# Kernel tuning notes

Hardware: AMD Instinct MI355X
Metric: run time of the kernel (lower is better)

## Reference

```python
import jax, jax.numpy as jnp
import numpy as np

N = 100000          # nodes
E = 1600000         # directed edges (avg degree 16)
DIMS = [256, 256, 256, 128]


def setup_inputs() -> dict:
    key = jax.random.key(0)
    ks = jax.random.split(key, 3 + 2 * (len(DIMS) - 1))
    X = jax.random.normal(ks[0], (N, DIMS[0]), dtype=jnp.float32)
    row = jax.random.randint(ks[1], (E,), 0, N, dtype=jnp.int32)
    col = jax.random.randint(ks[2], (E,), 0, N, dtype=jnp.int32)
    inp = {"X": X, "row": row, "col": col}
    # LinearLayer params: weights ~ N(0,1)/sqrt(in_features), bias = 0
    for i in range(len(DIMS) - 1):
        d_in, d_out = DIMS[i], DIMS[i + 1]
        inp[f"W{i}"] = jax.random.normal(ks[3 + i], (d_out, d_in), dtype=jnp.float32) / jnp.sqrt(d_in)
        inp[f"b{i}"] = jnp.zeros((d_out,), dtype=jnp.float32)
    return inp


def reference(X, row, col, W0, b0, W1, b1, W2, b2):
    n = X.shape[0]
    # normalized_adjacency: A' = I + A, then D^{-1/2} A' D^{-1/2}
    loop = jnp.arange(n, dtype=row.dtype)
    rows = jnp.concatenate([row, loop])          # [E+N]
    cols = jnp.concatenate([col, loop])          # [E+N]
    vals = jnp.ones(rows.shape[0], dtype=X.dtype)
    deg = jax.ops.segment_sum(vals, rows, num_segments=n)   # row sums of A'
    norm = vals / (jnp.sqrt(deg[rows]) * jnp.sqrt(deg[cols]))  # [E+N]

    def spmm(H):  # S @ H via gather + scatter-add
        return jax.ops.segment_sum(norm[:, None] * H[cols], rows, num_segments=n)

    H = spmm(X)
    H = jax.nn.gelu(H @ W0.T + b0)
    H = spmm(H)
    H = jax.nn.gelu(H @ W1.T + b1)
    H = spmm(H)
    H = H @ W2.T + b2  # final_non_linearity = identity
    return H
```

## Files before the change

### kernel.cpp

```cpp
#include <hip/hip_runtime.h>
#include <hip/hip_bf16.h>


typedef float f32x4 __attribute__((ext_vector_type(4)));
typedef float f32x2 __attribute__((ext_vector_type(2)));
typedef _Float16 h16x8 __attribute__((ext_vector_type(8)));
typedef _Float16 h16x4 __attribute__((ext_vector_type(4)));

__device__ __forceinline__ float gelu_fast(float x) {
    float u = 0.7978845608028654f * (x + 0.044715f * x * x * x);
    return x / (1.0f + __expf(-2.0f * u));
}

__global__ void count_kernel(const int* __restrict__ row, int* __restrict__ cnt,
                             int* __restrict__ rank, int e) {
    int i = blockIdx.x * blockDim.x + threadIdx.x;
    if (i < e) rank[i] = atomicAdd(&cnt[row[i]], 1);
}

__global__ void rnorm_kernel(const int* __restrict__ cnt, float* __restrict__ rnorm, int n) {
    int i = blockIdx.x * blockDim.x + threadIdx.x;
    if (i < n) rnorm[i] = rsqrtf((float)(cnt[i] + 1));
}

__global__ void scan1_kernel(const int* __restrict__ cnt, int* __restrict__ rowptr,
                             int* __restrict__ bsum, int n) {
    __shared__ int s[1024];
    int t = threadIdx.x;
    int i = blockIdx.x * 1024 + t;
    int v = (i < n) ? cnt[i] : 0;
    s[t] = v;
    __syncthreads();
    for (int off = 1; off < 1024; off <<= 1) {
        int x = (t >= off) ? s[t - off] : 0;
        __syncthreads();
        s[t] += x;
        __syncthreads();
    }
    if (i < n) rowptr[i] = s[t] - v;
    if (t == 1023) bsum[blockIdx.x] = s[1023];
}

__global__ void scan2_kernel(int* bsum, int nb) {
    __shared__ int s[128];
    int t = threadIdx.x;
    int v = (t < nb) ? bsum[t] : 0;
    s[t] = v;
    __syncthreads();
    for (int off = 1; off < 128; off <<= 1) {
        int x = (t >= off) ? s[t - off] : 0;
        __syncthreads();
        s[t] += x;
        __syncthreads();
    }
    if (t < nb) bsum[t] = s[t] - v;
}

__global__ void scan3_kernel(int* __restrict__ rowptr, const int* __restrict__ bsum, int n, int e) {
    int i = blockIdx.x * blockDim.x + threadIdx.x;
    if (i < n) rowptr[i] += bsum[i >> 10];
    if (i == 0) rowptr[n] = e;
}

__global__ void fill_kernel(const int* __restrict__ row, const int* __restrict__ col,
                            const int* __restrict__ rank,
                            const int* __restrict__ rowptr,
                            const float* __restrict__ rnorm,
                            int2* __restrict__ meta, int e) {
    int i = blockIdx.x * blockDim.x + threadIdx.x;
    if (i >= e) return;
    int r = row[i], c = col[i];
    int pos = rowptr[r] + rank[i];
    float w = rnorm[r] * rnorm[c];
    meta[pos] = make_int2(c, __float_as_int(w));
}

__global__ void splitW_kernel(const float* __restrict__ in,
                              _Float16* __restrict__ hi,
                              _Float16* __restrict__ lo, int total4) {
    int i = blockIdx.x * blockDim.x + threadIdx.x;
    if (i >= total4) return;
    f32x4 x = *(const f32x4*)(in + (size_t)i * 4);
    h16x4 h, l;
#pragma unroll
    for (int q = 0; q < 4; ++q) {
        _Float16 hb = (_Float16)x[q];
        h[q] = hb;
        l[q] = (_Float16)(x[q] - (float)hb);
    }
    *(h16x4*)(hi + (size_t)i * 4) = h;
    *(h16x4*)(lo + (size_t)i * 4) = l;
}

template <int D, bool GELU, bool SPLIT>
__global__ __launch_bounds__(256) void spmm_kernel(const _Float16* __restrict__ in,
                                                   float* __restrict__ out,
                                                   _Float16* __restrict__ oat,
                                                   const int* __restrict__ rowptr,
                                                   const int2* __restrict__ meta,
                                                   const float* __restrict__ rnorm,
                                                   const float* __restrict__ bias, int n) {
    constexpr int LPR = D / 8;
    constexpr int RPW = 64 / LPR;
    constexpr int BR = 4 * RPW;
    __shared__ _Float16 h_lds[8][256];

    int t = threadIdx.x;
    int lane = t & 63;
    int w = t >> 6;
    int sub = lane % LPR;
    int rowsel = lane / LPR;
    int wid = blockIdx.x * BR + w * RPW + rowsel;
    if (wid >= n) wid = n - 1;

    const _Float16* lanebase = in + sub * 8;
    float rn = rnorm[wid];
    float sw = rn * rn;
    float acc[8];
    {
        h16x8 a = *(const h16x8*)(lanebase + (size_t)wid * D);
#pragma unroll
        for (int q = 0; q < 8; ++q) acc[q] = sw * (float)a[q];
    }

    int e0 = rowptr[wid], e1 = rowptr[wid + 1];
    int ne = e1 - e0;
    int maxb = (ne + 3) >> 2;
    int elast = (e1 > e0) ? (e1 - 1) : 0;

    int2 m[4];
    auto loadM = [&](int b) {
#pragma unroll
        for (int u = 0; u < 4; ++u) {
            int idx = e0 + b * 4 + u;
            int eu = idx < e1 ? idx : elast;
            int2 mm = meta[eu];
            if (idx >= e1) mm.y = 0;
            m[u] = mm;
        }
    };
    if (maxb > 0) loadM(0);
    for (int b = 0; b < maxb; ++b) {
        h16x8 v[4];
#pragma unroll
        for (int u = 0; u < 4; ++u)
            v[u] = *(const h16x8*)(lanebase + (size_t)m[u].x * D);
        float wts[4];
#pragma unroll
        for (int u = 0; u < 4; ++u) wts[u] = __int_as_float(m[u].y);
        if (b + 1 < maxb) loadM(b + 1);
#pragma unroll
        for (int u = 0; u < 4; ++u)
#pragma unroll
            for (int q = 0; q < 8; ++q) acc[q] = fmaf(wts[u], (float)v[u][q], acc[q]);
    }

    if (SPLIT) {
        f32x4 bv0 = *(const f32x4*)(bias + sub * 8);
        f32x4 bv1 = *(const f32x4*)(bias + sub * 8 + 4);
        h16x8 h;
#pragma unroll
        for (int q = 0; q < 4; ++q) {
            float x0 = acc[q] + bv0[q];
            float x1 = acc[q + 4] + bv1[q];
            h[q] = (_Float16)(GELU ? gelu_fast(x0) : x0);
            h[q + 4] = (_Float16)(GELU ? gelu_fast(x1) : x1);
        }
        *(h16x8*)&h_lds[w * 2 + rowsel][sub * 8] = h;
        __syncthreads();
        int kc = t >> 5;
        int g  = (t >> 3) & 3;
        int j  = t & 7;
        size_t rg = (size_t)(blockIdx.x >> 1);
        int half = blockIdx.x & 1;
        size_t toff = ((rg * 8 + kc) * 64 + g * 16 + half * 8 + j) * 8;
        __builtin_nontemporal_store(*(const h16x8*)&h_lds[j][kc * 32 + g * 8],
                                    (h16x8*)(oat + toff));
    } else {
        f32x4 bv0 = *(const f32x4*)(bias + sub * 8);
        f32x4 bv1 = *(const f32x4*)(bias + sub * 8 + 4);
        f32x4 o0, o1;
#pragma unroll
        for (int q = 0; q < 4; ++q) {
            float x0 = acc[q] + bv0[q];
            float x1 = acc[q + 4] + bv1[q];
            o0[q] = GELU ? gelu_fast(x0) : x0;
            o1[q] = GELU ? gelu_fast(x1) : x1;
        }
        float* dst = out + (size_t)wid * D + sub * 8;
        __builtin_nontemporal_store(o0, (f32x4*)dst);
        __builtin_nontemporal_store(o1, (f32x4*)(dst + 4));
    }
}

template <int DO, int RT, bool XIN>
__global__ __launch_bounds__(256, 2) void dense_mfma_kernel(
        const _Float16* __restrict__ AT, const float* __restrict__ Xf,
        const _Float16* __restrict__ Whi, const _Float16* __restrict__ Wlo,
        _Float16* __restrict__ out, int n) {
    constexpr int KC = 32;
    constexpr int NCH = 256 / KC;
    constexpr int NTT = DO / 16;
    constexpr int NT = NTT / 2;
    constexpr int NFRAG = 2 * NTT;
    constexpr int BM = 2 * RT * 16;
    __shared__ h16x8 s_w[2][NFRAG * 64];

    int t = threadIdx.x;
    int lane = t & 63;
    int w = t >> 6;
    int r = lane & 15;
    int g = lane >> 4;
    int h = w & 1;
    int row0 = blockIdx.x * BM + (w >> 1) * (RT * 16);
    int n16 = (n + 15) >> 4;

    size_t argi[RT];
#pragma unroll
    for (int rt = 0; rt < RT; ++rt) {
        if (XIN) {
            int arow = row0 + rt * 16 + r;
            if (arow >= n) arow = n - 1;
            argi[rt] = (size_t)arow;
        } else {
            int rg = (row0 >> 4) + rt;
            if (rg >= n16) rg = n16 - 1;
            argi[rt] = (size_t)rg;
        }
    }

    f32x4 acc[RT][NT];
#pragma unroll
    for (int rt = 0; rt < RT; ++rt)
#pragma unroll
        for (int nt = 0; nt < NT; ++nt) acc[rt][nt] = (f32x4){0.f, 0.f, 0.f, 0.f};

    auto stage = [&](int c, int b) {
#pragma unroll
        for (int i = 0; i < NFRAG / 4; ++i) {
            int s = t + i * 256;
            int sl = s & 63;
            int f = s >> 6;
            int ntf = f % NTT;
            int op = f / NTT;
            const _Float16* src = op ? Wlo : Whi;
            const _Float16* gsrc =
                &src[(size_t)(ntf * 16 + (sl & 15)) * 256 + c * KC + ((sl >> 4) << 3)];
            __builtin_amdgcn_global_load_lds(
                (const __attribute__((address_space(1))) void*)gsrc,
                (__attribute__((address_space(3))) void*)&s_w[b][s], 16, 0, 0);
        }
    };

    h16x8 aC[2][RT];
    f32x4 nf[RT][2];

    auto prefetchA = [&](int c, int set) {
#pragma unroll
        for (int rt = 0; rt < RT; ++rt) {
            if (XIN) {
                const float* src = &Xf[argi[rt] * 256 + c * KC + g * 8];
                nf[rt][0] = *(const f32x4*)src;
                nf[rt][1] = *(const f32x4*)(src + 4);
            } else {
                aC[set][rt] = *(const h16x8*)&AT[((argi[rt] * 8 + c) * 64 + lane) * 8];
            }
        }
    };
    auto commitA = [&](int set) {
        if (XIN) {
#pragma unroll
            for (int rt = 0; rt < RT; ++rt) {
                h16x8 hh;
#pragma unroll
                for (int q = 0; q < 4; ++q) {
                    hh[q] = (_Float16)nf[rt][0][q];
                    hh[q + 4] = (_Float16)nf[rt][1][q];
                }
                aC[set][rt] = hh;
            }
        }
    };

    stage(0, 0);
    prefetchA(0, 0);
    asm volatile("s_waitcnt vmcnt(0)" ::: "memory");
    __builtin_amdgcn_sched_barrier(0);
    commitA(0);
    __builtin_amdgcn_s_barrier();
    __builtin_amdgcn_sched_barrier(0);

#pragma unroll
    for (int c = 0; c < NCH; ++c) {
        const int b = c & 1;
        if (c + 1 < NCH) {
            stage(c + 1, b ^ 1);
            prefetchA(c + 1, b ^ 1);
            constexpr int VM = (NFRAG / 4) + (XIN ? 2 * RT : RT);
            asm volatile("s_waitcnt vmcnt(%0)" :: "i"(VM) : "memory");
        } else {
            asm volatile("s_waitcnt vmcnt(0)" ::: "memory");
        }
        __builtin_amdgcn_sched_barrier(0);
        __builtin_amdgcn_s_barrier();
        __builtin_amdgcn_sched_barrier(0);

#pragma unroll
        for (int nt = 0; nt < NT; ++nt) {
            int ntf = h * NT + nt;
            h16x8 wh = s_w[b][ntf * 64 + lane];
            h16x8 wl = s_w[b][(NTT + ntf) * 64 + lane];
#pragma unroll
            for (int rt = 0; rt < RT; ++rt) {
                acc[rt][nt] = __builtin_amdgcn_mfma_f32_16x16x32_f16(aC[b][rt], wh, acc[rt][nt], 0, 0, 0);
                acc[rt][nt] = __builtin_amdgcn_mfma_f32_16x16x32_f16(aC[b][rt], wl, acc[rt][nt], 0, 0, 0);
            }
        }
        __builtin_amdgcn_sched_barrier(0);
        if (c + 1 < NCH) commitA(b ^ 1);
        __builtin_amdgcn_s_barrier();
    }

#pragma unroll
    for (int rt = 0; rt < RT; ++rt) {
#pragma unroll
        for (int nt = 0; nt < NT; ++nt) {
            int ccol = (h * NT + nt) * 16 + r;
#pragma unroll
            for (int j = 0; j < 4; ++j) {
                int rr = row0 + rt * 16 + g * 4 + j;
                if (rr < n) out[(size_t)rr * DO + ccol] = (_Float16)acc[rt][nt][j];
            }
        }
    }
}

extern "C" void kernel_launch(void* const* d_in, const int* in_sizes, int n_in,
                              void* d_out, int out_size, void* d_ws, size_t ws_size,
                              hipStream_t stream) {
    const float* X  = (const float*)d_in[0];
    const int* row  = (const int*)d_in[1];
    const int* col  = (const int*)d_in[2];
    const float* W0 = (const float*)d_in[3];
    const float* b0 = (const float*)d_in[4];
    const float* W1 = (const float*)d_in[5];
    const float* b1 = (const float*)d_in[6];
    const float* W2 = (const float*)d_in[7];
    const float* b2 = (const float*)d_in[8];

    int n = in_sizes[0] / 256;
    int e = in_sizes[1];
    size_t n16pad = (size_t)((n + 15) / 16) * 16;

    char* ws = (char*)d_ws;
    size_t off = 0;
    auto alloc = [&](size_t bytes) {
        void* p = ws + off;
        off += (bytes + 255) & ~(size_t)255;
        return p;
    };
    _Float16* AT  = (_Float16*)alloc(n16pad * 256 * 2);
    _Float16* Dh  = (_Float16*)alloc((size_t)n * 256 * 2);
    _Float16* W0h = (_Float16*)alloc(256 * 256 * 2);
    _Float16* W0l = (_Float16*)alloc(256 * 256 * 2);
    _Float16* W1h = (_Float16*)alloc(256 * 256 * 2);
    _Float16* W1l = (_Float16*)alloc(256 * 256 * 2);
    _Float16* W2h = (_Float16*)alloc(256 * 128 * 2);
    _Float16* W2l = (_Float16*)alloc(256 * 128 * 2);
    int*   cnt    = (int*)alloc((size_t)n * 4);
    int*   rank   = (int*)alloc((size_t)e * 4);
    float* rnorm  = (float*)alloc((size_t)n * 4);
    int*   rowptr = (int*)alloc(((size_t)n + 1) * 4);
    int*   bsum   = (int*)alloc(512);
    int2*  meta   = (int2*)alloc((size_t)e * 8);

    (void)hipMemsetAsync(cnt, 0, (size_t)n * 4, stream);

    int gE = (e + 255) / 256;
    int gN = (n + 255) / 256;
    int nb = (n + 1023) / 1024;

    count_kernel<<<gE, 256, 0, stream>>>(row, cnt, rank, e);
    rnorm_kernel<<<gN, 256, 0, stream>>>(cnt, rnorm, n);
    scan1_kernel<<<nb, 1024, 0, stream>>>(cnt, rowptr, bsum, n);
    scan2_kernel<<<1, 128, 0, stream>>>(bsum, nb);
    scan3_kernel<<<gN, 256, 0, stream>>>(rowptr, bsum, n, e);
    fill_kernel<<<gE, 256, 0, stream>>>(row, col, rank, rowptr, rnorm, meta, e);

    splitW_kernel<<<(16384 + 255) / 256, 256, 0, stream>>>(W0, W0h, W0l, 16384);
    splitW_kernel<<<(16384 + 255) / 256, 256, 0, stream>>>(W1, W1h, W1l, 16384);
    splitW_kernel<<<(8192 + 255) / 256, 256, 0, stream>>>(W2, W2h, W2l, 8192);

    int gS  = (n + 7) / 8;
    int gS2 = (n + 15) / 16;
    int gMd = (n + 127) / 128;

    dense_mfma_kernel<256, 4, true><<<gMd, 256, 0, stream>>>(nullptr, X, W0h, W0l, Dh, n);
    spmm_kernel<256, true, true><<<gS, 256, 0, stream>>>(Dh, nullptr, AT, rowptr, meta, rnorm, b0, n);
    dense_mfma_kernel<256, 4, false><<<gMd, 256, 0, stream>>>(AT, nullptr, W1h, W1l, Dh, n);
    spmm_kernel<256, true, true><<<gS, 256, 0, stream>>>(Dh, nullptr, AT, rowptr, meta, rnorm, b1, n);
    dense_mfma_kernel<128, 4, false><<<gMd, 256, 0, stream>>>(AT, nullptr, W2h, W2l, Dh, n);
    spmm_kernel<128, false, false><<<gS2, 256, 0, stream>>>(Dh, (float*)d_out, nullptr, rowptr, meta, rnorm, b2, n);
}
```

Before: 574.0 us.

## Factor symmetric normalization out of edges, store only column indices

Splits the edge weight rnorm[r]*rnorm[c] so the column factor is applied in the dense GEMM epilogue and the row factor in the SpMM epilogue. The per-edge metadata shrinks from an int2 (column plus weight) to a bare column index, halving metadata traffic in each SpMM. The rnorm computation moves into scan1 and the three weight-split launches merge into one, removing several small launches. Padding is added to rnorm and AT so the vectorized rnorm read past n stays in bounds, and results change slightly because fp16 values are now rounded after scaling.

```diff
diff --git a/kernel.cpp b/kernel.cpp
--- a/kernel.cpp
+++ b/kernel.cpp
@@ -18,17 +18,13 @@
     if (i < e) rank[i] = atomicAdd(&cnt[row[i]], 1);
 }
 
-__global__ void rnorm_kernel(const int* __restrict__ cnt, float* __restrict__ rnorm, int n) {
-    int i = blockIdx.x * blockDim.x + threadIdx.x;
-    if (i < n) rnorm[i] = rsqrtf((float)(cnt[i] + 1));
-}
-
 __global__ void scan1_kernel(const int* __restrict__ cnt, int* __restrict__ rowptr,
-                             int* __restrict__ bsum, int n) {
+                             int* __restrict__ bsum, float* __restrict__ rnorm, int n) {
     __shared__ int s[1024];
     int t = threadIdx.x;
     int i = blockIdx.x * 1024 + t;
     int v = (i < n) ? cnt[i] : 0;
+    if (i < n) rnorm[i] = rsqrtf((float)(v + 1));
     s[t] = v;
     __syncthreads();
     for (int off = 1; off < 1024; off <<= 1) {
@@ -65,22 +61,25 @@
 __global__ void fill_kernel(const int* __restrict__ row, const int* __restrict__ col,
                             const int* __restrict__ rank,
                             const int* __restrict__ rowptr,
-                            const float* __restrict__ rnorm,
-                            int2* __restrict__ meta, int e) {
+                            int* __restrict__ metac, int e) {
     int i = blockIdx.x * blockDim.x + threadIdx.x;
     if (i >= e) return;
-    int r = row[i], c = col[i];
-    int pos = rowptr[r] + rank[i];
-    float w = rnorm[r] * rnorm[c];
-    meta[pos] = make_int2(c, __float_as_int(w));
-}
-
-__global__ void splitW_kernel(const float* __restrict__ in,
-                              _Float16* __restrict__ hi,
-                              _Float16* __restrict__ lo, int total4) {
+    metac[rowptr[row[i]] + rank[i]] = col[i];
+}
+
+__global__ void splitW_kernel(const float* __restrict__ W0, const float* __restrict__ W1,
+                              const float* __restrict__ W2,
+                              _Float16* __restrict__ W0h, _Float16* __restrict__ W0l,
+                              _Float16* __restrict__ W1h, _Float16* __restrict__ W1l,
+                              _Float16* __restrict__ W2h, _Float16* __restrict__ W2l) {
     int i = blockIdx.x * blockDim.x + threadIdx.x;
-    if (i >= total4) return;
-    f32x4 x = *(const f32x4*)(in + (size_t)i * 4);
+    const float* src;
+    _Float16 *dh, *dl;
+    int j;
+    if (i < 16384)      { src = W0; dh = W0h; dl = W0l; j = i; }
+    else if (i < 32768) { src = W1; dh = W1h; dl = W1l; j = i - 16384; }
+    else                { src = W2; dh = W2h; dl = W2l; j = i - 32768; }
+    f32x4 x = *(const f32x4*)(src + (size_t)j * 4);
     h16x4 h, l;
 #pragma unroll
     for (int q = 0; q < 4; ++q) {
@@ -88,8 +87,8 @@
         h[q] = hb;
         l[q] = (_Float16)(x[q] - (float)hb);
     }
-    *(h16x4*)(hi + (size_t)i * 4) = h;
-    *(h16x4*)(lo + (size_t)i * 4) = l;
+    *(h16x4*)(dh + (size_t)j * 4) = h;
+    *(h16x4*)(dl + (size_t)j * 4) = l;
 }
 
 template <int D, bool GELU, bool SPLIT>
@@ -97,7 +96,7 @@
                                                    float* __restrict__ out,
                                                    _Float16* __restrict__ oat,
                                                    const int* __restrict__ rowptr,
-                                                   const int2* __restrict__ meta,
+                                                   const int* __restrict__ metac,
                                                    const float* __restrict__ rnorm,
                                                    const float* __restrict__ bias, int n) {
     constexpr int LPR = D / 8;
@@ -115,12 +114,11 @@
 
     const _Float16* lanebase = in + sub * 8;
     float rn = rnorm[wid];
-    float sw = rn * rn;
     float acc[8];
     {
         h16x8 a = *(const h16x8*)(lanebase + (size_t)wid * D);
 #pragma unroll
-        for (int q = 0; q < 8; ++q) acc[q] = sw * (float)a[q];
+        for (int q = 0; q < 8; ++q) acc[q] = (float)a[q];
     }
 
     int e0 = rowptr[wid], e1 = rowptr[wid + 1];
@@ -128,15 +126,15 @@
     int maxb = (ne + 3) >> 2;
     int elast = (e1 > e0) ? (e1 - 1) : 0;
 
-    int2 m[4];
+    int mc[4];
+    float mw[4];
     auto loadM = [&](int b) {
 #pragma unroll
         for (int u = 0; u < 4; ++u) {
             int idx = e0 + b * 4 + u;
-            int eu = idx < e1 ? idx : elast;
-            int2 mm = meta[eu];
-            if (idx >= e1) mm.y = 0;
-            m[u] = mm;
+            bool val = idx < e1;
+            mc[u] = metac[val ? idx : elast];
+            mw[u] = val ? 1.0f : 0.0f;
         }
     };
     if (maxb > 0) loadM(0);
@@ -144,10 +142,10 @@
         h16x8 v[4];
 #pragma unroll
         for (int u = 0; u < 4; ++u)
-            v[u] = *(const h16x8*)(lanebase + (size_t)m[u].x * D);
+            v[u] = *(const h16x8*)(lanebase + (size_t)mc[u] * D);
         float wts[4];
 #pragma unroll
-        for (int u = 0; u < 4; ++u) wts[u] = __int_as_float(m[u].y);
+        for (int u = 0; u < 4; ++u) wts[u] = mw[u];
         if (b + 1 < maxb) loadM(b + 1);
 #pragma unroll
         for (int u = 0; u < 4; ++u)
@@ -161,8 +159,8 @@
         h16x8 h;
 #pragma unroll
         for (int q = 0; q < 4; ++q) {
-            float x0 = acc[q] + bv0[q];
-            float x1 = acc[q + 4] + bv1[q];
+            float x0 = acc[q] * rn + bv0[q];
+            float x1 = acc[q + 4] * rn + bv1[q];
             h[q] = (_Float16)(GELU ? gelu_fast(x0) : x0);
             h[q + 4] = (_Float16)(GELU ? gelu_fast(x1) : x1);
         }
@@ -182,8 +180,8 @@
         f32x4 o0, o1;
 #pragma unroll
         for (int q = 0; q < 4; ++q) {
-            float x0 = acc[q] + bv0[q];
-            float x1 = acc[q + 4] + bv1[q];
+            float x0 = acc[q] * rn + bv0[q];
+            float x1 = acc[q + 4] * rn + bv1[q];
             o0[q] = GELU ? gelu_fast(x0) : x0;
             o1[q] = GELU ? gelu_fast(x1) : x1;
         }
@@ -197,6 +195,7 @@
 __global__ __launch_bounds__(256, 2) void dense_mfma_kernel(
         const _Float16* __restrict__ AT, const float* __restrict__ Xf,
         const _Float16* __restrict__ Whi, const _Float16* __restrict__ Wlo,
+        const float* __restrict__ rnorm,
         _Float16* __restrict__ out, int n) {
     constexpr int KC = 32;
     constexpr int NCH = 256 / KC;
@@ -323,13 +322,14 @@
 
 #pragma unroll
     for (int rt = 0; rt < RT; ++rt) {
+        f32x4 rn4 = *(const f32x4*)&rnorm[row0 + rt * 16 + g * 4];
 #pragma unroll
         for (int nt = 0; nt < NT; ++nt) {
             int ccol = (h * NT + nt) * 16 + r;
 #pragma unroll
             for (int j = 0; j < 4; ++j) {
                 int rr = row0 + rt * 16 + g * 4 + j;
-                if (rr < n) out[(size_t)rr * DO + ccol] = (_Float16)acc[rt][nt][j];
+                if (rr < n) out[(size_t)rr * DO + ccol] = (_Float16)(acc[rt][nt][j] * rn4[j]);
             }
         }
     }
@@ -350,7 +350,7 @@
 
     int n = in_sizes[0] / 256;
     int e = in_sizes[1];
-    size_t n16pad = (size_t)((n + 15) / 16) * 16;
+    size_t n16pad = (size_t)((n + 15) / 16) * 16 + 128;
 
     char* ws = (char*)d_ws;
     size_t off = 0;
@@ -369,10 +369,10 @@
     _Float16* W2l = (_Float16*)alloc(256 * 128 * 2);
     int*   cnt    = (int*)alloc((size_t)n * 4);
     int*   rank   = (int*)alloc((size_t)e * 4);
-    float* rnorm  = (float*)alloc((size_t)n * 4);
+    float* rnorm  = (float*)alloc((size_t)n * 4 + 1024);
     int*   rowptr = (int*)alloc(((size_t)n + 1) * 4);
     int*   bsum   = (int*)alloc(512);
-    int2*  meta   = (int2*)alloc((size_t)e * 8);
+    int*   metac  = (int*)alloc((size_t)e * 4);
 
     (void)hipMemsetAsync(cnt, 0, (size_t)n * 4, stream);
 
@@ -381,24 +381,20 @@
     int nb = (n + 1023) / 1024;
 
     count_kernel<<<gE, 256, 0, stream>>>(row, cnt, rank, e);
-    rnorm_kernel<<<gN, 256, 0, stream>>>(cnt, rnorm, n);
-    scan1_kernel<<<nb, 1024, 0, stream>>>(cnt, rowptr, bsum, n);
+    scan1_kernel<<<nb, 1024, 0, stream>>>(cnt, rowptr, bsum, rnorm, n);
     scan2_kernel<<<1, 128, 0, stream>>>(bsum, nb);
     scan3_kernel<<<gN, 256, 0, stream>>>(rowptr, bsum, n, e);
-    fill_kernel<<<gE, 256, 0, stream>>>(row, col, rank, rowptr, rnorm, meta, e);
-
-    splitW_kernel<<<(16384 + 255) / 256, 256, 0, stream>>>(W0, W0h, W0l, 16384);
-    splitW_kernel<<<(16384 + 255) / 256, 256, 0, stream>>>(W1, W1h, W1l, 16384);
-    splitW_kernel<<<(8192 + 255) / 256, 256, 0, stream>>>(W2, W2h, W2l, 8192);
+    fill_kernel<<<gE, 256, 0, stream>>>(row, col, rank, rowptr, metac, e);
+    splitW_kernel<<<40960 / 256, 256, 0, stream>>>(W0, W1, W2, W0h, W0l, W1h, W1l, W2h, W2l);
 
     int gS  = (n + 7) / 8;
     int gS2 = (n + 15) / 16;
     int gMd = (n + 127) / 128;
 
-    dense_mfma_kernel<256, 4, true><<<gMd, 256, 0, stream>>>(nullptr, X, W0h, W0l, Dh, n);
-    spmm_kernel<256, true, true><<<gS, 256, 0, stream>>>(Dh, nullptr, AT, rowptr, meta, rnorm, b0, n);
-    dense_mfma_kernel<256, 4, false><<<gMd, 256, 0, stream>>>(AT, nullptr, W1h, W1l, Dh, n);
-    spmm_kernel<256, true, true><<<gS, 256, 0, stream>>>(Dh, nullptr, AT, rowptr, meta, rnorm, b1, n);
-    dense_mfma_kernel<128, 4, false><<<gMd, 256, 0, stream>>>(AT, nullptr, W2h, W2l, Dh, n);
-    spmm_kernel<128, false, false><<<gS2, 256, 0, stream>>>(Dh, (float*)d_out, nullptr, rowptr, meta, rnorm, b2, n);
-}
+    dense_mfma_kernel<256, 4, true><<<gMd, 256, 0, stream>>>(nullptr, X, W0h, W0l, rnorm, Dh, n);
+    spmm_kernel<256, true, true><<<gS, 256, 0, stream>>>(Dh, nullptr, AT, rowptr, metac, rnorm, b0, n);
+    dense_mfma_kernel<256, 4, false><<<gMd, 256, 0, stream>>>(AT, nullptr, W1h, W1l, rnorm, Dh, n);
+    spmm_kernel<256, true, true><<<gS, 256, 0, stream>>>(Dh, nullptr, AT, rowptr, metac, rnorm, b1, n);
+    dense_mfma_kernel<128, 4, false><<<gMd, 256, 0, stream>>>(AT, nullptr, W2h, W2l, rnorm, Dh, n);
+    spmm_kernel<128, false, false><<<gS2, 256, 0, stream>>>(Dh, (float*)d_out, nullptr, rowptr, metac, rnorm, b2, n);
+}
```

After: 621.2 us. +8.2%, slower.
